# Kernel tuning notes

Measured on AMD Instinct MI355X. Metric: run time of the kernel, lower is better.

The kernel has to match this reference:

```python
import jax, jax.numpy as jnp
import numpy as np

DIM, WIDTH, POOL, BATCH, SEQ = 4096, 4, 512, 256, 16

def setup_inputs() -> dict:
    key = jax.random.key(0)
    k1, k2, k3, k4 = jax.random.split(key, 4)
    x = jax.random.normal(k1, (BATCH, SEQ, DIM), dtype=jnp.float32)
    conv_state = jax.random.normal(k2, (POOL, WIDTH - 1, DIM), dtype=jnp.float32)
    weight = jax.random.normal(k3, (WIDTH, DIM), dtype=jnp.float32)
    bias = jax.random.normal(k4, (DIM,), dtype=jnp.float32)
    conv_state_indices = jnp.arange(BATCH, dtype=jnp.int32)
    return {"x": x, "conv_state": conv_state, "weight": weight,
            "bias": bias, "conv_state_indices": conv_state_indices}

def reference(x, conv_state, weight, bias, conv_state_indices):
    # x: [b, s, d]; conv_state: [pool, width-1, d]; weight: [width, d]
    b, s, d = x.shape
    width = weight.shape[0]
    state = conv_state[conv_state_indices]            # gather: [b, width-1, d]
    x_new = jnp.concatenate([state, x], axis=1)       # [b, width-1+s, d]
    # depthwise causal conv, width taps (small fixed loop over taps)
    out = bias
    for k in range(width):
        out = out + x_new[:, k:k + s, :] * weight[k]  # [b, s, d]
    out = jax.nn.silu(out)                            # activation=True
    new_state = x_new[:, -(width - 1):, :]            # [b, width-1, d]
    updated_conv_state = conv_state.at[conv_state_indices].set(new_state)
    return out, updated_conv_state
```

## Files before the change

### kernel.cpp

```cpp
#include <hip/hip_runtime.h>

constexpr int DIM   = 4096;
constexpr int WIDTH = 4;
constexpr int POOL  = 512;
constexpr int BATCH = 256;
constexpr int SEQ   = 16;

constexpr int D4_CHUNKS    = DIM / (4 * 256);
constexpr int CONV_BLOCKS  = D4_CHUNKS * BATCH;
constexpr int TOTAL_BLOCKS = CONV_BLOCKS + POOL;

typedef float f32x4 __attribute__((ext_vector_type(4)));

__device__ __forceinline__ f32x4 ld4(const float* p) {
    return *reinterpret_cast<const f32x4*>(p);
}
__device__ __forceinline__ f32x4 ld4_nt(const float* p) {
    return __builtin_nontemporal_load(reinterpret_cast<const f32x4*>(p));
}
__device__ __forceinline__ void st4_nt(float* p, f32x4 v) {
    __builtin_nontemporal_store(v, reinterpret_cast<f32x4*>(p));
}

__global__ __launch_bounds__(256) void fused_conv_update_kernel(
    const float* __restrict__ x,
    const float* __restrict__ conv_state,
    const float* __restrict__ weight,
    const float* __restrict__ bias,
    const int*   __restrict__ idxs,
    float*       __restrict__ out,
    float*       __restrict__ out_state)
{
    const int blk = blockIdx.x;

    if (blk < CONV_BLOCKS) {
        const int b     = blk >> 2;
        const int chunk = blk & (D4_CHUNKS - 1);
        const int d     = (chunk * 256 + threadIdx.x) * 4;
        const int idx   = idxs[b];

        const float* xb = x + (size_t)b * SEQ * DIM + d;
        const float* st = conv_state + (size_t)idx * (WIDTH - 1) * DIM + d;

        f32x4 win0 = ld4(st + 0 * DIM);
        f32x4 win1 = ld4(st + 1 * DIM);
        f32x4 win2 = ld4(st + 2 * DIM);
        f32x4 xcur = ld4_nt(xb);

        const f32x4 w0 = ld4(weight + 0 * DIM + d);
        const f32x4 w1 = ld4(weight + 1 * DIM + d);
        const f32x4 w2 = ld4(weight + 2 * DIM + d);
        const f32x4 w3 = ld4(weight + 3 * DIM + d);
        const f32x4 bs = ld4(bias + d);

        float* ob = out + (size_t)b * SEQ * DIM + d;

#pragma unroll
        for (int s = 0; s < SEQ; ++s) {
            f32x4 xnext;
            if (s + 1 < SEQ) xnext = ld4_nt(xb + (size_t)(s + 1) * DIM);

            f32x4 acc = bs + win0 * w0 + win1 * w1 + win2 * w2 + xcur * w3;

            acc.x = acc.x / (1.0f + expf(-acc.x));
            acc.y = acc.y / (1.0f + expf(-acc.y));
            acc.z = acc.z / (1.0f + expf(-acc.z));
            acc.w = acc.w / (1.0f + expf(-acc.w));

            st4_nt(ob + (size_t)s * DIM, acc);

            win0 = win1; win1 = win2; win2 = xcur;
            if (s + 1 < SEQ) xcur = xnext;
        }

        float* sd = out_state + (size_t)idx * (WIDTH - 1) * DIM + d;
        st4_nt(sd + 0 * DIM, win0);
        st4_nt(sd + 1 * DIM, win1);
        st4_nt(sd + 2 * DIM, win2);
    } else {
        const int row = blk - CONV_BLOCKS;

        __shared__ int skip;
        if (threadIdx.x == 0) skip = 0;
        __syncthreads();
        if (idxs[threadIdx.x] == row) skip = 1;
        __syncthreads();
        if (skip) return;

        const float* src = conv_state + (size_t)row * (WIDTH - 1) * DIM;
        float*       dst = out_state  + (size_t)row * (WIDTH - 1) * DIM;

        constexpr int ROW_F4 = (WIDTH - 1) * DIM / 4;
#pragma unroll
        for (int i = threadIdx.x; i < ROW_F4; i += 256)
            st4_nt(dst + (size_t)i * 4, ld4_nt(src + (size_t)i * 4));
    }
}

extern "C" void kernel_launch(void* const* d_in, const int* in_sizes, int n_in,
                              void* d_out, int out_size, void* d_ws, size_t ws_size,
                              hipStream_t stream)
{
    const float* x          = (const float*)d_in[0];
    const float* conv_state = (const float*)d_in[1];
    const float* weight     = (const float*)d_in[2];
    const float* bias       = (const float*)d_in[3];
    const int*   idxs       = (const int*)  d_in[4];

    float* out       = (float*)d_out;
    float* out_state = out + (size_t)BATCH * SEQ * DIM;

    fused_conv_update_kernel<<<TOTAL_BLOCKS, 256, 0, stream>>>(
        x, conv_state, weight, bias, idxs, out, out_state);
}
```

Before: 40.64 us.

## Merge pool-copy into conv blocks, preload all inputs, use fast SiLU

Removes the separate pool-copy blocks and has each conv block copy half of one pool row after finishing its convolution. All sequence inputs are loaded up front into registers behind a scheduling barrier to maximize memory-level parallelism. Nontemporal loads and stores are replaced with plain ones, and SiLU uses a fast exp and reciprocal. Register pressure rises, and the cache behaviour of ordinary stores may differ.

```diff
diff --git a/kernel.cpp b/kernel.cpp
--- a/kernel.cpp
+++ b/kernel.cpp
@@ -6,23 +6,22 @@
 constexpr int BATCH = 256;
 constexpr int SEQ   = 16;
 
-constexpr int D4_CHUNKS    = DIM / (4 * 256);
-constexpr int CONV_BLOCKS  = D4_CHUNKS * BATCH;
-constexpr int TOTAL_BLOCKS = CONV_BLOCKS + POOL;
+constexpr int D4_CHUNKS   = DIM / (4 * 256);
+constexpr int CONV_BLOCKS = D4_CHUNKS * BATCH;
 
 typedef float f32x4 __attribute__((ext_vector_type(4)));
 
 __device__ __forceinline__ f32x4 ld4(const float* p) {
     return *reinterpret_cast<const f32x4*>(p);
 }
-__device__ __forceinline__ f32x4 ld4_nt(const float* p) {
-    return __builtin_nontemporal_load(reinterpret_cast<const f32x4*>(p));
+__device__ __forceinline__ void st4(float* p, f32x4 v) {
+    *reinterpret_cast<f32x4*>(p) = v;
 }
-__device__ __forceinline__ void st4_nt(float* p, f32x4 v) {
-    __builtin_nontemporal_store(v, reinterpret_cast<f32x4*>(p));
+__device__ __forceinline__ float fast_silu(float v) {
+    return v * __builtin_amdgcn_rcpf(1.0f + __expf(-v));
 }
 
-__global__ __launch_bounds__(256) void fused_conv_update_kernel(
+__global__ __launch_bounds__(256, 4) void fused_conv_update_kernel(
     const float* __restrict__ x,
     const float* __restrict__ conv_state,
     const float* __restrict__ weight,
@@ -31,70 +30,67 @@
     float*       __restrict__ out,
     float*       __restrict__ out_state)
 {
-    const int blk = blockIdx.x;
+    const int blk   = blockIdx.x;
+    const int b     = blk >> 2;
+    const int chunk = blk & (D4_CHUNKS - 1);
+    const int d     = (chunk * 256 + threadIdx.x) * 4;
+    const int idx   = idxs[b];
 
-    if (blk < CONV_BLOCKS) {
-        const int b     = blk >> 2;
-        const int chunk = blk & (D4_CHUNKS - 1);
-        const int d     = (chunk * 256 + threadIdx.x) * 4;
-        const int idx   = idxs[b];
+    const float* xb = x + (size_t)b * SEQ * DIM + d;
+    const float* st = conv_state + (size_t)idx * (WIDTH - 1) * DIM + d;
 
-        const float* xb = x + (size_t)b * SEQ * DIM + d;
-        const float* st = conv_state + (size_t)idx * (WIDTH - 1) * DIM + d;
+    f32x4 xv[SEQ + WIDTH - 1];
+    xv[0] = ld4(st + 0 * DIM);
+    xv[1] = ld4(st + 1 * DIM);
+    xv[2] = ld4(st + 2 * DIM);
+#pragma unroll
+    for (int s = 0; s < SEQ; ++s)
+        xv[WIDTH - 1 + s] = ld4(xb + (size_t)s * DIM);
 
-        f32x4 win0 = ld4(st + 0 * DIM);
-        f32x4 win1 = ld4(st + 1 * DIM);
-        f32x4 win2 = ld4(st + 2 * DIM);
-        f32x4 xcur = ld4_nt(xb);
+    const f32x4 w0 = ld4(weight + 0 * DIM + d);
+    const f32x4 w1 = ld4(weight + 1 * DIM + d);
+    const f32x4 w2 = ld4(weight + 2 * DIM + d);
+    const f32x4 w3 = ld4(weight + 3 * DIM + d);
+    const f32x4 bs = ld4(bias + d);
 
-        const f32x4 w0 = ld4(weight + 0 * DIM + d);
-        const f32x4 w1 = ld4(weight + 1 * DIM + d);
-        const f32x4 w2 = ld4(weight + 2 * DIM + d);
-        const f32x4 w3 = ld4(weight + 3 * DIM + d);
-        const f32x4 bs = ld4(bias + d);
+    __builtin_amdgcn_sched_barrier(0);
 
-        float* ob = out + (size_t)b * SEQ * DIM + d;
+    float* ob = out + (size_t)b * SEQ * DIM + d;
+#pragma unroll
+    for (int s = 0; s < SEQ; ++s) {
+        f32x4 acc = bs + xv[s] * w0 + xv[s + 1] * w1 + xv[s + 2] * w2 + xv[s + 3] * w3;
+        acc.x = fast_silu(acc.x);
+        acc.y = fast_silu(acc.y);
+        acc.z = fast_silu(acc.z);
+        acc.w = fast_silu(acc.w);
+        st4(ob + (size_t)s * DIM, acc);
+    }
 
+    float* sd = out_state + (size_t)idx * (WIDTH - 1) * DIM + d;
+    st4(sd + 0 * DIM, xv[SEQ + 0]);
+    st4(sd + 1 * DIM, xv[SEQ + 1]);
+    st4(sd + 2 * DIM, xv[SEQ + 2]);
+
+    const int row     = blk >> 1;
+    const int halfsel = blk & 1;
+
+    __shared__ int skip;
+    if (threadIdx.x == 0) skip = 0;
+    __syncthreads();
+    if (idxs[threadIdx.x] == row) skip = 1;
+    __syncthreads();
+    if (skip) return;
+
+    constexpr int HALF_FLOATS = (WIDTH - 1) * DIM / 2;
+    const float* src = conv_state + (size_t)row * (WIDTH - 1) * DIM
+                     + (size_t)halfsel * HALF_FLOATS;
+    float* dst = out_state + (size_t)row * (WIDTH - 1) * DIM
+               + (size_t)halfsel * HALF_FLOATS;
+
+    constexpr int HALF_F4 = HALF_FLOATS / 4;
 #pragma unroll
-        for (int s = 0; s < SEQ; ++s) {
-            f32x4 xnext;
-            if (s + 1 < SEQ) xnext = ld4_nt(xb + (size_t)(s + 1) * DIM);
-
-            f32x4 acc = bs + win0 * w0 + win1 * w1 + win2 * w2 + xcur * w3;
-
-            acc.x = acc.x / (1.0f + expf(-acc.x));
-            acc.y = acc.y / (1.0f + expf(-acc.y));
-            acc.z = acc.z / (1.0f + expf(-acc.z));
-            acc.w = acc.w / (1.0f + expf(-acc.w));
-
-            st4_nt(ob + (size_t)s * DIM, acc);
-
-            win0 = win1; win1 = win2; win2 = xcur;
-            if (s + 1 < SEQ) xcur = xnext;
-        }
-
-        float* sd = out_state + (size_t)idx * (WIDTH - 1) * DIM + d;
-        st4_nt(sd + 0 * DIM, win0);
-        st4_nt(sd + 1 * DIM, win1);
-        st4_nt(sd + 2 * DIM, win2);
-    } else {
-        const int row = blk - CONV_BLOCKS;
-
-        __shared__ int skip;
-        if (threadIdx.x == 0) skip = 0;
-        __syncthreads();
-        if (idxs[threadIdx.x] == row) skip = 1;
-        __syncthreads();
-        if (skip) return;
-
-        const float* src = conv_state + (size_t)row * (WIDTH - 1) * DIM;
-        float*       dst = out_state  + (size_t)row * (WIDTH - 1) * DIM;
-
-        constexpr int ROW_F4 = (WIDTH - 1) * DIM / 4;
-#pragma unroll
-        for (int i = threadIdx.x; i < ROW_F4; i += 256)
-            st4_nt(dst + (size_t)i * 4, ld4_nt(src + (size_t)i * 4));
-    }
+    for (int i = threadIdx.x; i < HALF_F4; i += 256)
+        st4(dst + (size_t)i * 4, ld4(src + (size_t)i * 4));
 }
 
 extern "C" void kernel_launch(void* const* d_in, const int* in_sizes, int n_in,
@@ -110,6 +106,6 @@
     float* out       = (float*)d_out;
     float* out_state = out + (size_t)BATCH * SEQ * DIM;
 
-    fused_conv_update_kernel<<<TOTAL_BLOCKS, 256, 0, stream>>>(
+    fused_conv_update_kernel<<<CONV_BLOCKS, 256, 0, stream>>>(
         x, conv_state, weight, bias, idxs, out, out_state);
 }
```

New measurement: 32.53 us. -20.0%, faster.
